# Kernel optimization log

Measured on AMD Instinct MI355X. Metric: run time of the kernel, lower is better.

## Reference

```python
import jax, jax.numpy as jnp
import numpy as np

ATT = 128  # attention_size
D = 128    # entity_embedding_dim


def setup_inputs() -> dict:
    key = jax.random.key(0)
    k1, k2, k3, k4, k5 = jax.random.split(key, 5)
    B, N, K = 1024, 50, 5
    entity_embedding = jax.random.normal(k1, (B, N, D), dtype=jnp.float32)
    neigh_entity_embedding = jax.random.normal(k2, (B, N, K, D), dtype=jnp.float32)
    neigh_relation_embedding = jax.random.normal(k3, (B, N, K, D), dtype=jnp.float32)
    # fc1: Linear(3*D -> ATT), fc2: Linear(ATT -> 1)
    lim1 = 1.0 / np.sqrt(3 * D)
    lim2 = 1.0 / np.sqrt(ATT)
    W1 = jax.random.uniform(k4, (3 * D, ATT), minval=-lim1, maxval=lim1, dtype=jnp.float32)
    b1 = jnp.zeros((ATT,), dtype=jnp.float32)
    W2 = jax.random.uniform(k5, (ATT, 1), minval=-lim2, maxval=lim2, dtype=jnp.float32)
    b2 = jnp.zeros((1,), dtype=jnp.float32)
    return {
        "entity_embedding": entity_embedding,
        "neigh_entity_embedding": neigh_entity_embedding,
        "neigh_relation_embedding": neigh_relation_embedding,
        "W1": W1, "b1": b1, "W2": W2, "b2": b2,
    }


def reference(entity_embedding, neigh_entity_embedding, neigh_relation_embedding, W1, b1, W2, b2):
    B, N, K, Dd = neigh_entity_embedding.shape
    # expand entity to each of the K neighbors: [B, N, K, D]
    ent_exp = jnp.broadcast_to(entity_embedding[:, :, None, :], (B, N, K, Dd))
    # concat along feature dim -> [B, N, K, 3D]
    concat = jnp.concatenate([ent_exp, neigh_entity_embedding, neigh_relation_embedding], axis=3)
    # tiny MLP: fc1 -> fc2 gives one logit per neighbor
    h = jnp.einsum('bnkf,fa->bnka', concat, W1) + b1          # [B, N, K, ATT]
    logits = jnp.einsum('bnka,ao->bnko', h, W2) + b2          # [B, N, K, 1]
    att = jax.nn.softmax(logits, axis=2)                      # softmax over K neighbors
    neigh_att = jnp.sum(att * neigh_entity_embedding, axis=2) # [B, N, D]
    # squeeze() on [B,N,D] with no singleton dims is identity
    return jnp.concatenate([entity_embedding, neigh_att], axis=-1)  # [B, N, 2D]
```

## Files before the change

### kernel.cpp

```cpp
#include <hip/hip_runtime.h>
#include <math.h>


#define DIM 128
#define KN 5

typedef float nfloat4 __attribute__((ext_vector_type(4)));

__device__ __forceinline__ float dot4(nfloat4 a, nfloat4 b) {
    return a.x * b.x + a.y * b.y + a.z * b.z + a.w * b.w;
}

__global__ __launch_bounds__(256) void kgat_prep(
    const float* __restrict__ W1,
    const float* __restrict__ b1,
    const float* __restrict__ W2,
    const float* __restrict__ b2,
    float* __restrict__ ws)
{
    const int gw = blockIdx.x * 4 + (threadIdx.x >> 6);
    const int lane = threadIdx.x & 63;
    if (gw < 3 * DIM) {
        const int t = gw;
        const float2 w1 = *(const float2*)(W1 + (size_t)t * DIM + 2 * lane);
        const float2 w2 = *(const float2*)(W2 + 2 * lane);
        float v = w1.x * w2.x + w1.y * w2.y;
        #pragma unroll
        for (int off = 32; off >= 1; off >>= 1) v += __shfl_xor(v, off, 64);
        if (lane == 0) ws[t] = v;
    } else if (gw == 3 * DIM) {
        const float2 bb = *(const float2*)(b1 + 2 * lane);
        const float2 w2 = *(const float2*)(W2 + 2 * lane);
        float v = bb.x * w2.x + bb.y * w2.y;
        #pragma unroll
        for (int off = 32; off >= 1; off >>= 1) v += __shfl_xor(v, off, 64);
        if (lane == 0) ws[3 * DIM] = v + b2[0];
    }
}

#define LOAD_ROW(pp, e4, n4, r4)                                            \
    do {                                                                    \
        e4 = *(const nfloat4*)(ent + (size_t)(pp) * DIM + d);               \
        const size_t rowK_ = (size_t)(pp) * (KN * DIM) + d;                 \
        _Pragma("unroll")                                                   \
        for (int k = 0; k < KN; ++k) {                                      \
            n4[k] = *(const nfloat4*)(ne + rowK_ + (size_t)k * DIM);        \
            r4[k] = *(const nfloat4*)(nr + rowK_ + (size_t)k * DIM);        \
        }                                                                   \
    } while (0)

#define PROCESS_ROW(pc, e4, n4, r4)                                         \
    do {                                                                    \
        float red[KN];                                                      \
        const float ec = dot4(e4, we);                                      \
        _Pragma("unroll")                                                   \
        for (int k = 0; k < KN; ++k)                                        \
            red[k] = ec + dot4(n4[k], wne) + dot4(r4[k], wnr);              \
        _Pragma("unroll")                                                   \
        for (int j = 0; j < KN; ++j) {                                      \
            float v = red[j];                                               \
            _Pragma("unroll")                                               \
            for (int off = 16; off >= 1; off >>= 1)                         \
                v += __shfl_xor(v, off, 64);                                \
            red[j] = v;                                                     \
        }                                                                   \
        float m = red[0];                                                   \
        _Pragma("unroll")                                                   \
        for (int k = 1; k < KN; ++k) m = fmaxf(m, red[k]);                  \
        float ex[KN], s = 0.f;                                              \
        _Pragma("unroll")                                                   \
        for (int k = 0; k < KN; ++k) { ex[k] = __expf(red[k] - m); s += ex[k]; } \
        const float inv = 1.f / s;                                          \
        nfloat4 acc = {0.f, 0.f, 0.f, 0.f};                                 \
        _Pragma("unroll")                                                   \
        for (int k = 0; k < KN; ++k) {                                      \
            const float a = ex[k] * inv;                                    \
            acc.x += a * n4[k].x;                                           \
            acc.y += a * n4[k].y;                                           \
            acc.z += a * n4[k].z;                                           \
            acc.w += a * n4[k].w;                                           \
        }                                                                   \
        float* orow_ = out + (size_t)(pc) * (2 * DIM);                      \
        __builtin_nontemporal_store(e4,  (nfloat4*)(orow_ + d));            \
        __builtin_nontemporal_store(acc, (nfloat4*)(orow_ + DIM + d));      \
    } while (0)

__global__ __launch_bounds__(256, 4) void kgat_main(
    const float* __restrict__ ent,
    const float* __restrict__ ne,
    const float* __restrict__ nr,
    const float* __restrict__ ws,
    float* __restrict__ out,
    int P, int L)
{
    const int wave = threadIdx.x >> 6;
    const int lane = threadIdx.x & 63;
    const int half = lane >> 5;
    const int l    = lane & 31;
    const int d    = l * 4;
    const int h    = wave * 2 + half;

    const int base = blockIdx.x * (8 * L);
    int pend = base + 8 * L;
    if (pend > P) pend = P;
    int p = base + h;
    if (p >= pend) return;

    const nfloat4 we  = *(const nfloat4*)(ws + d);
    const nfloat4 wne = *(const nfloat4*)(ws + DIM + d);
    const nfloat4 wnr = *(const nfloat4*)(ws + 2 * DIM + d);

    nfloat4 eA, neA[KN], nrA[KN];
    nfloat4 eB, neB[KN], nrB[KN];

    LOAD_ROW(p, eA, neA, nrA);
    int pn = p + 8;

    for (;;) {
        if (pn < pend) LOAD_ROW(pn, eB, neB, nrB);
        __builtin_amdgcn_sched_barrier(0);
        PROCESS_ROW(p, eA, neA, nrA);
        p = pn;
        if (p >= pend) break;
        pn = p + 8;

        if (pn < pend) LOAD_ROW(pn, eA, neA, nrA);
        __builtin_amdgcn_sched_barrier(0);
        PROCESS_ROW(p, eB, neB, nrB);
        p = pn;
        if (p >= pend) break;
        pn = p + 8;
    }
}

extern "C" void kernel_launch(void* const* d_in, const int* in_sizes, int n_in,
                              void* d_out, int out_size, void* d_ws, size_t ws_size,
                              hipStream_t stream) {
    const float* ent = (const float*)d_in[0];
    const float* ne  = (const float*)d_in[1];
    const float* nr  = (const float*)d_in[2];
    const float* W1  = (const float*)d_in[3];
    const float* b1  = (const float*)d_in[4];
    const float* W2  = (const float*)d_in[5];
    const float* b2  = (const float*)d_in[6];
    float* out = (float*)d_out;
    float* ws  = (float*)d_ws;

    const int P = in_sizes[0] / DIM;

    kgat_prep<<<(3 * DIM + 1 + 3) / 4, 256, 0, stream>>>(W1, b1, W2, b2, ws);

    int L = (P + 8 * 1024 - 1) / (8 * 1024);
    if (L < 1) L = 1;
    int nb = (P + 8 * L - 1) / (8 * L);
    if (nb < 1) nb = 1;
    kgat_main<<<nb, 256, 0, stream>>>(ent, ne, nr, ws, out, P, L);
}
```

Before: 330.3 us.

## Replace persistent double-buffered row loop with one-shot two-rows-per-half-wave grid

Drops the persistent-style loop, where each block walked many rows with a software-pipelined A/B register double buffer, and launches one block per 16 rows instead. Each half-wave now loads two adjacent rows up front, processes both, and writes them out. The aim is to expose more memory-level parallelism through a much larger grid and to remove loop and branch overhead, relying on hardware wave scheduling instead of manual prefetch. Occupancy is pinned to 4 waves per EU. The trade-off is losing the explicit load/compute overlap within a wave and paying more block launch overhead.

```diff
diff --git a/kernel.cpp b/kernel.cpp
--- a/kernel.cpp
+++ b/kernel.cpp
@@ -49,7 +49,7 @@
         }                                                                   \
     } while (0)
 
-#define PROCESS_ROW(pc, e4, n4, r4)                                         \
+#define PROCESS_ROW(e4, n4, r4, acc)                                        \
     do {                                                                    \
         float red[KN];                                                      \
         const float ec = dot4(e4, we);                                      \
@@ -71,7 +71,6 @@
         _Pragma("unroll")                                                   \
         for (int k = 0; k < KN; ++k) { ex[k] = __expf(red[k] - m); s += ex[k]; } \
         const float inv = 1.f / s;                                          \
-        nfloat4 acc = {0.f, 0.f, 0.f, 0.f};                                 \
         _Pragma("unroll")                                                   \
         for (int k = 0; k < KN; ++k) {                                      \
             const float a = ex[k] * inv;                                    \
@@ -80,56 +79,50 @@
             acc.z += a * n4[k].z;                                           \
             acc.w += a * n4[k].w;                                           \
         }                                                                   \
-        float* orow_ = out + (size_t)(pc) * (2 * DIM);                      \
-        __builtin_nontemporal_store(e4,  (nfloat4*)(orow_ + d));            \
-        __builtin_nontemporal_store(acc, (nfloat4*)(orow_ + DIM + d));      \
     } while (0)
 
-__global__ __launch_bounds__(256, 4) void kgat_main(
+__global__ __launch_bounds__(256)
+__attribute__((amdgpu_waves_per_eu(4, 4)))
+void kgat_main(
     const float* __restrict__ ent,
     const float* __restrict__ ne,
     const float* __restrict__ nr,
     const float* __restrict__ ws,
     float* __restrict__ out,
-    int P, int L)
+    int P)
 {
     const int wave = threadIdx.x >> 6;
     const int lane = threadIdx.x & 63;
     const int half = lane >> 5;
     const int l    = lane & 31;
     const int d    = l * 4;
-    const int h    = wave * 2 + half;
 
-    const int base = blockIdx.x * (8 * L);
-    int pend = base + 8 * L;
-    if (pend > P) pend = P;
-    int p = base + h;
-    if (p >= pend) return;
+    const int p0 = blockIdx.x * 16 + (wave * 2 + half) * 2;
+    if (p0 >= P) return;
+    const int p1 = p0 + 1;
+    const int p1c = (p1 < P) ? p1 : p0;
 
     const nfloat4 we  = *(const nfloat4*)(ws + d);
     const nfloat4 wne = *(const nfloat4*)(ws + DIM + d);
     const nfloat4 wnr = *(const nfloat4*)(ws + 2 * DIM + d);
 
-    nfloat4 eA, neA[KN], nrA[KN];
-    nfloat4 eB, neB[KN], nrB[KN];
+    nfloat4 e0, n0[KN], r0[KN];
+    nfloat4 e1, n1[KN], r1[KN];
+    LOAD_ROW(p0,  e0, n0, r0);
+    LOAD_ROW(p1c, e1, n1, r1);
 
-    LOAD_ROW(p, eA, neA, nrA);
-    int pn = p + 8;
+    nfloat4 acc0 = {0.f, 0.f, 0.f, 0.f};
+    nfloat4 acc1 = {0.f, 0.f, 0.f, 0.f};
+    PROCESS_ROW(e0, n0, r0, acc0);
+    PROCESS_ROW(e1, n1, r1, acc1);
 
-    for (;;) {
-        if (pn < pend) LOAD_ROW(pn, eB, neB, nrB);
-        __builtin_amdgcn_sched_barrier(0);
-        PROCESS_ROW(p, eA, neA, nrA);
-        p = pn;
-        if (p >= pend) break;
-        pn = p + 8;
-
-        if (pn < pend) LOAD_ROW(pn, eA, neA, nrA);
-        __builtin_amdgcn_sched_barrier(0);
-        PROCESS_ROW(p, eB, neB, nrB);
-        p = pn;
-        if (p >= pend) break;
-        pn = p + 8;
+    float* orow0 = out + (size_t)p0 * (2 * DIM);
+    __builtin_nontemporal_store(e0,   (nfloat4*)(orow0 + d));
+    __builtin_nontemporal_store(acc0, (nfloat4*)(orow0 + DIM + d));
+    if (p1 < P) {
+        float* orow1 = out + (size_t)p1 * (2 * DIM);
+        __builtin_nontemporal_store(e1,   (nfloat4*)(orow1 + d));
+        __builtin_nontemporal_store(acc1, (nfloat4*)(orow1 + DIM + d));
     }
 }
 
@@ -150,9 +143,6 @@
 
     kgat_prep<<<(3 * DIM + 1 + 3) / 4, 256, 0, stream>>>(W1, b1, W2, b2, ws);
 
-    int L = (P + 8 * 1024 - 1) / (8 * 1024);
-    if (L < 1) L = 1;
-    int nb = (P + 8 * L - 1) / (8 * L);
-    if (nb < 1) nb = 1;
-    kgat_main<<<nb, 256, 0, stream>>>(ent, ne, nr, ws, out, P, L);
+    const int nb = (P + 15) / 16;
+    kgat_main<<<nb, 256, 0, stream>>>(ent, ne, nr, ws, out, P);
 }
```

New measurement: 314.5 us. -4.8%, faster.
